# Kernel tuning notes

Hardware: AMD Instinct MI355X
Metric: run time of the kernel (lower is better)

## Reference

```python
import jax, jax.numpy as jnp
import numpy as np

N_NODES, N_EDGES, B, K, D = 200000, 500000, 8192, 32, 128
E_DIM, E_EMB, N_CLASS = 128, 128, 60


def setup_inputs() -> dict:
    key = jax.random.key(0)
    ks = jax.random.split(key, 16)
    s = lambda k, shape, scale=0.05: jax.random.normal(k, shape, dtype=jnp.float32) * scale
    return {
        'memory_emb': s(ks[0], (N_NODES, D), 1.0),
        'edge_feat': s(ks[1], (N_EDGES, E_DIM), 1.0),
        'W_q': s(ks[2], (D, D)),
        'W_k': s(ks[3], (D, D)),
        'a': s(ks[4], (2 * D,)),
        'We_w': s(ks[5], (E_DIM, E_EMB)),
        'We_b': s(ks[6], (E_EMB,)),
        'Wuc': s(ks[7], (D + 2 * D + E_EMB, D)),
        'Wc1': s(ks[8], (D, 128)),
        'Wc2': s(ks[9], (128, N_CLASS)),
        'src_idxs': jax.random.randint(ks[10], (B,), 0, N_NODES),
        'dst_idxs': jax.random.randint(ks[11], (B,), 0, N_NODES),
        'edge_idxs': jax.random.randint(ks[12], (B,), 0, N_EDGES),
        'src_neighbors': jax.random.randint(ks[13], (B, K), 0, N_NODES),
        'dst_neighbors': jax.random.randint(ks[14], (B, K), 0, N_NODES),
    }


def reference(memory_emb, edge_feat, W_q, W_k, a, We_w, We_b, Wuc, Wc1, Wc2,
              src_idxs, dst_idxs, edge_idxs, src_neighbors, dst_neighbors):
    def attend(idxs, nbrs):
        self_emb = memory_emb[idxs]                      # [B, D] gather
        nb = memory_emb[nbrs]                            # [B, K, D] gather
        q = self_emb @ W_q                               # [B, D]
        k = jnp.einsum('bkd,de->bke', nb, W_k)           # [B, K, D]
        # GAT-style score: leaky_relu(a . [q || k])
        sq = q @ a[:D]                                   # [B]
        sk = jnp.einsum('bkd,d->bk', k, a[D:])           # [B, K]
        score = jax.nn.leaky_relu(sq[:, None] + sk, 0.2)
        attn = jax.nn.softmax(score, axis=-1)            # [B, K]
        agg = jnp.einsum('bk,bkd->bd', attn, k)          # [B, D]
        return self_emb, agg

    src_e, src_h = attend(src_idxs, src_neighbors)
    dst_e, dst_h = attend(dst_idxs, dst_neighbors)
    e = edge_feat[edge_idxs] @ We_w + We_b               # edge embedding [B, E_EMB]
    msg_src = jax.nn.relu(jnp.concatenate([src_e, src_h, dst_h, e], -1) @ Wuc)
    msg_dst = jax.nn.relu(jnp.concatenate([dst_e, dst_h, src_h, e], -1) @ Wuc)
    logits_src = jax.nn.relu(msg_src @ Wc1) @ Wc2
    logits_dst = jax.nn.relu(msg_dst @ Wc1) @ Wc2
    return jnp.stack([logits_src, logits_dst])           # [2, B, N_CLASS]
```

## Files before the change

kernel.cpp:

```cpp
#include <hip/hip_runtime.h>

#define D 128
#define KNBR 32
#define BATCH 8192
#define NCLASS 60
#define NB 16
#define NP 32

__global__ __launch_bounds__(256) void k_prep(
    const float* __restrict__ Wq, const float* __restrict__ Wk,
    const float* __restrict__ a, const float* __restrict__ Wew,
    const float* __restrict__ Web, const float* __restrict__ Wuc,
    float* __restrict__ wqa, float* __restrict__ wka,
    float* __restrict__ be, float* __restrict__ Wcomb2)
{
    __shared__ float sB[128][129];
    int blk = blockIdx.x, tid = threadIdx.x;
    if (blk == 0) {
        for (int t = tid; t < 128 * 128; t += 256) sB[t >> 7][t & 127] = Wq[t];
        __syncthreads();
        if (tid < 128) {
            float s = 0.f;
            for (int j = 0; j < D; ++j) s += sB[tid][j] * a[j];
            wqa[tid] = s;
        }
        __syncthreads();
        for (int t = tid; t < 128 * 128; t += 256) sB[t >> 7][t & 127] = Wk[t];
        __syncthreads();
        if (tid < 128) {
            float s = 0.f;
            for (int j = 0; j < D; ++j) s += sB[tid][j] * a[D + j];
            wka[tid] = s;
        }
    } else if (blk == 1) {
        if (tid < 128) {
            float acc = 0.f;
            for (int j = 0; j < D; ++j) acc += Web[j] * Wuc[(size_t)(384 + j) * D + tid];
            be[tid] = acc;
        }
    } else {
        int g  = (blk - 2) >> 4;
        int rb = ((blk - 2) & 15) * 8;
        const float* A = (g == 2) ? Wew : Wk;
        const float* B = Wuc + (size_t)(128 + g * 128) * D;
        for (int t = tid; t < 128 * 128; t += 256) sB[t >> 7][t & 127] = B[t];
        __syncthreads();
        int j = tid & 127, half = tid >> 7;
        float acc[4] = {0.f, 0.f, 0.f, 0.f};
        int r0 = rb + half * 4;
        for (int t = 0; t < 128; ++t) {
            float bv = sB[t][j];
            #pragma unroll
            for (int m = 0; m < 4; ++m)
                acc[m] = fmaf(A[(size_t)(r0 + m) * D + t], bv, acc[m]);
        }
        #pragma unroll
        for (int m = 0; m < 4; ++m)
            Wcomb2[(size_t)(g * 128 + r0 + m) * D + j] = acc[m];
    }
}

__global__ __launch_bounds__(256) void k_scores(
    const float* __restrict__ mem,
    const float* __restrict__ wqa, const float* __restrict__ wka,
    float* __restrict__ nsq, float* __restrict__ nsk)
{
    int tid = threadIdx.x, lane = tid & 31, grp = tid >> 5;
    int n0 = blockIdx.x * 64 + grp * 8;
    float4 wq4 = ((const float4*)wqa)[lane];
    float4 wk4 = ((const float4*)wka)[lane];
    #pragma unroll
    for (int i = 0; i < 8; ++i) {
        int n = n0 + i;
        float4 v = ((const float4*)(mem + (size_t)n * D))[lane];
        float pq = v.x * wq4.x + v.y * wq4.y + v.z * wq4.z + v.w * wq4.w;
        float pk = v.x * wk4.x + v.y * wk4.y + v.z * wk4.z + v.w * wk4.w;
        #pragma unroll
        for (int m = 1; m <= 16; m <<= 1) {
            pq += __shfl_xor(pq, m, 32);
            pk += __shfl_xor(pk, m, 32);
        }
        if (lane == 0) nsq[n] = pq;
        if (lane == 1) nsk[n] = pk;
    }
}

__global__ __launch_bounds__(256, 3) void k_fused(
    const float* __restrict__ mem, const float* __restrict__ edge_feat,
    const float* __restrict__ Wuc, const float* __restrict__ Wcomb2,
    const float* __restrict__ be,
    const float* __restrict__ nsq, const float* __restrict__ nsk,
    const float* __restrict__ Wc1, const float* __restrict__ Wc2,
    const int* __restrict__ src_idxs, const int* __restrict__ dst_idxs,
    const int* __restrict__ edge_idxs,
    const int* __restrict__ src_nb, const int* __restrict__ dst_nb,
    float* __restrict__ out)
{
    __shared__ __align__(16) float Ws[32 * 128];
    __shared__ __align__(16) float nbT[128 * 33];
    __shared__ __align__(16) float uni[128 * 33];
    __shared__ int s_sidx[NP];
    __shared__ int s_eidx[NB];

    int tid = threadIdx.x;
    int b0 = blockIdx.x * NB;
    int lane = tid & 31;
    int grp  = tid >> 5;

    if (tid < NP) s_sidx[tid] = ((tid >> 4) ? dst_idxs : src_idxs)[b0 + (tid & 15)];
    if (tid < NB) s_eidx[tid] = edge_idxs[b0 + tid];

    for (int it = 0; it < 4; ++it) {
        int p = it * 8 + grp;
        int side = p >> 4;
        int bb = b0 + (p & 15);
        int self_idx = (side ? dst_idxs : src_idxs)[bb];
        int ik = (side ? dst_nb : src_nb)[(size_t)bb * KNBR + lane];

        float x = nsq[self_idx] + nsk[ik];
        x = (x >= 0.f) ? x : 0.2f * x;
        float mx = x;
        #pragma unroll
        for (int m = 1; m <= 16; m <<= 1) mx = fmaxf(mx, __shfl_xor(mx, m, 32));
        float e = __expf(x - mx);
        float sum = e;
        #pragma unroll
        for (int m = 1; m <= 16; m <<= 1) sum += __shfl_xor(sum, m, 32);
        float attn = e / sum;

        float4 acc = make_float4(0.f, 0.f, 0.f, 0.f);
        #pragma unroll 8
        for (int k = 0; k < KNBR; ++k) {
            int ikk  = __shfl(ik, k, 32);
            float ak = __shfl(attn, k, 32);
            float4 v = ((const float4*)(mem + (size_t)ikk * D))[lane];
            acc.x = fmaf(ak, v.x, acc.x);
            acc.y = fmaf(ak, v.y, acc.y);
            acc.z = fmaf(ak, v.z, acc.z);
            acc.w = fmaf(ak, v.w, acc.w);
        }
        nbT[(lane * 4 + 0) * 33 + p] = acc.x;
        nbT[(lane * 4 + 1) * 33 + p] = acc.y;
        nbT[(lane * 4 + 2) * 33 + p] = acc.z;
        nbT[(lane * 4 + 3) * 33 + p] = acc.w;
    }
    __syncthreads();

    int tr = tid >> 4, tc = tid & 15;
    int lc = tid & 31, lr = tid >> 5;
    int wc = tid & 127, wk2 = tid >> 7;
    float accB[2][8];
    #pragma unroll
    for (int i = 0; i < 2; ++i)
        #pragma unroll
        for (int j = 0; j < 8; ++j) accB[i][j] = 0.f;

    float* Ast = uni;

    for (int kt = 0; kt < 4; ++kt) {
        int off = kt * 32;
        #pragma unroll
        for (int q = 0; q < 4; ++q) {
            int r = lr + 8 * q;
            Ast[lc * 33 + r] = mem[(size_t)s_sidx[r] * D + off + lc];
        }
        #pragma unroll
        for (int pp = 0; pp < 16; ++pp) {
            int kk = wk2 + 2 * pp;
            Ws[kk * 128 + wc] = Wuc[(size_t)(off + kk) * D + wc];
        }
        __syncthreads();
        #pragma unroll 8
        for (int kk = 0; kk < 32; ++kk) {
            float a0 = Ast[kk * 33 + tr * 2];
            float a1 = Ast[kk * 33 + tr * 2 + 1];
            float4 w0 = *(const float4*)&Ws[kk * 128 + tc * 4];
            float4 w1 = *(const float4*)&Ws[kk * 128 + 64 + tc * 4];
            float wr[8] = {w0.x, w0.y, w0.z, w0.w, w1.x, w1.y, w1.z, w1.w};
            #pragma unroll
            for (int j = 0; j < 8; ++j) {
                accB[0][j] = fmaf(a0, wr[j], accB[0][j]);
                accB[1][j] = fmaf(a1, wr[j], accB[1][j]);
            }
        }
        __syncthreads();
    }
    for (int kt = 4; kt < 12; ++kt) {
        int off = (kt & 3) * 32;
        int gr0 = kt * 32 - 128;
        #pragma unroll
        for (int pp = 0; pp < 16; ++pp) {
            int kk = wk2 + 2 * pp;
            Ws[kk * 128 + wc] = Wcomb2[(size_t)(gr0 + kk) * D + wc];
        }
        __syncthreads();
        int r0 = (kt < 8) ? (tr * 2) : ((tr * 2) ^ 16);
        #pragma unroll 8
        for (int kk = 0; kk < 32; ++kk) {
            float a0 = nbT[(off + kk) * 33 + r0];
            float a1 = nbT[(off + kk) * 33 + r0 + 1];
            float4 w0 = *(const float4*)&Ws[kk * 128 + tc * 4];
            float4 w1 = *(const float4*)&Ws[kk * 128 + 64 + tc * 4];
            float wr[8] = {w0.x, w0.y, w0.z, w0.w, w1.x, w1.y, w1.z, w1.w};
            #pragma unroll
            for (int j = 0; j < 8; ++j) {
                accB[0][j] = fmaf(a0, wr[j], accB[0][j]);
                accB[1][j] = fmaf(a1, wr[j], accB[1][j]);
            }
        }
        __syncthreads();
    }
    for (int kt = 12; kt < 16; ++kt) {
        int off = (kt & 3) * 32;
        int gr0 = kt * 32 - 128;
        #pragma unroll
        for (int q = 0; q < 4; ++q) {
            int r = lr + 8 * q;
            Ast[lc * 33 + r] = edge_feat[(size_t)s_eidx[r & 15] * D + off + lc];
        }
        #pragma unroll
        for (int pp = 0; pp < 16; ++pp) {
            int kk = wk2 + 2 * pp;
            Ws[kk * 128 + wc] = Wcomb2[(size_t)(gr0 + kk) * D + wc];
        }
        __syncthreads();
        #pragma unroll 8
        for (int kk = 0; kk < 32; ++kk) {
            float a0 = Ast[kk * 33 + tr * 2];
            float a1 = Ast[kk * 33 + tr * 2 + 1];
            float4 w0 = *(const float4*)&Ws[kk * 128 + tc * 4];
            float4 w1 = *(const float4*)&Ws[kk * 128 + 64 + tc * 4];
            float wr[8] = {w0.x, w0.y, w0.z, w0.w, w1.x, w1.y, w1.z, w1.w};
            #pragma unroll
            for (int j = 0; j < 8; ++j) {
                accB[0][j] = fmaf(a0, wr[j], accB[0][j]);
                accB[1][j] = fmaf(a1, wr[j], accB[1][j]);
            }
        }
        __syncthreads();
    }

    float* msgT = uni;
    {
        float4 bv0 = *(const float4*)&be[tc * 4];
        float4 bv1 = *(const float4*)&be[64 + tc * 4];
        float b8[8] = {bv0.x, bv0.y, bv0.z, bv0.w, bv1.x, bv1.y, bv1.z, bv1.w};
        #pragma unroll
        for (int i = 0; i < 2; ++i) {
            int r = tr * 2 + i;
            #pragma unroll
            for (int j = 0; j < 4; ++j) {
                msgT[(tc * 4 + j) * 33 + r]      = fmaxf(accB[i][j] + b8[j], 0.f);
                msgT[(64 + tc * 4 + j) * 33 + r] = fmaxf(accB[i][j + 4] + b8[j + 4], 0.f);
            }
        }
    }
    __syncthreads();

    float accC[2][8];
    #pragma unroll
    for (int i = 0; i < 2; ++i)
        #pragma unroll
        for (int j = 0; j < 8; ++j) accC[i][j] = 0.f;

    for (int kt = 0; kt < 4; ++kt) {
        int off = kt * 32;
        #pragma unroll
        for (int pp = 0; pp < 16; ++pp) {
            int kk = wk2 + 2 * pp;
            Ws[kk * 128 + wc] = Wc1[(size_t)(off + kk) * D + wc];
        }
        __syncthreads();
        #pragma unroll 8
        for (int kk = 0; kk < 32; ++kk) {
            float a0 = msgT[(off + kk) * 33 + tr * 2];
            float a1 = msgT[(off + kk) * 33 + tr * 2 + 1];
            float4 w0 = *(const float4*)&Ws[kk * 128 + tc * 4];
            float4 w1 = *(const float4*)&Ws[kk * 128 + 64 + tc * 4];
            float wr[8] = {w0.x, w0.y, w0.z, w0.w, w1.x, w1.y, w1.z, w1.w};
            #pragma unroll
            for (int j = 0; j < 8; ++j) {
                accC[0][j] = fmaf(a0, wr[j], accC[0][j]);
                accC[1][j] = fmaf(a1, wr[j], accC[1][j]);
            }
        }
        __syncthreads();
    }
    #pragma unroll
    for (int i = 0; i < 2; ++i) {
        int r = tr * 2 + i;
        #pragma unroll
        for (int j = 0; j < 4; ++j) {
            msgT[(tc * 4 + j) * 33 + r]      = fmaxf(accC[i][j], 0.f);
            msgT[(64 + tc * 4 + j) * 33 + r] = fmaxf(accC[i][j + 4], 0.f);
        }
    }
    __syncthreads();

    int r2 = tid & 31;
    int cs = tid >> 5;
    float acc2[8];
    #pragma unroll
    for (int j = 0; j < 8; ++j) acc2[j] = 0.f;

    for (int kt = 0; kt < 4; ++kt) {
        int off = kt * 32;
        for (int t = tid; t < 32 * 64; t += 256) {
            int kk = t >> 6, c = t & 63;
            Ws[t] = (c < NCLASS) ? Wc2[(size_t)(off + kk) * NCLASS + c] : 0.f;
        }
        __syncthreads();
        #pragma unroll 4
        for (int kk = 0; kk < 32; ++kk) {
            float h = msgT[(off + kk) * 33 + r2];
            float4 w0 = *(const float4*)&Ws[kk * 64 + cs * 8];
            float4 w1 = *(const float4*)&Ws[kk * 64 + cs * 8 + 4];
            acc2[0] = fmaf(h, w0.x, acc2[0]);
            acc2[1] = fmaf(h, w0.y, acc2[1]);
            acc2[2] = fmaf(h, w0.z, acc2[2]);
            acc2[3] = fmaf(h, w0.w, acc2[3]);
            acc2[4] = fmaf(h, w1.x, acc2[4]);
            acc2[5] = fmaf(h, w1.y, acc2[5]);
            acc2[6] = fmaf(h, w1.z, acc2[6]);
            acc2[7] = fmaf(h, w1.w, acc2[7]);
        }
        __syncthreads();
    }
    {
        int side = r2 >> 4;
        int bb = b0 + (r2 & 15);
        size_t orow = ((size_t)side * BATCH + bb) * NCLASS;
        #pragma unroll
        for (int j = 0; j < 8; ++j) {
            int c = cs * 8 + j;
            if (c < NCLASS) out[orow + c] = acc2[j];
        }
    }
}

extern "C" void kernel_launch(void* const* d_in, const int* in_sizes, int n_in,
                              void* d_out, int out_size, void* d_ws, size_t ws_size,
                              hipStream_t stream) {
    const float* mem       = (const float*)d_in[0];
    const float* edge_feat = (const float*)d_in[1];
    const float* Wq        = (const float*)d_in[2];
    const float* Wk        = (const float*)d_in[3];
    const float* a         = (const float*)d_in[4];
    const float* Wew       = (const float*)d_in[5];
    const float* Web       = (const float*)d_in[6];
    const float* Wuc       = (const float*)d_in[7];
    const float* Wc1       = (const float*)d_in[8];
    const float* Wc2       = (const float*)d_in[9];
    const int* src_idxs    = (const int*)d_in[10];
    const int* dst_idxs    = (const int*)d_in[11];
    const int* edge_idxs   = (const int*)d_in[12];
    const int* src_nb      = (const int*)d_in[13];
    const int* dst_nb      = (const int*)d_in[14];
    float* out = (float*)d_out;

    float* ws = (float*)d_ws;
    float* Wcomb2 = ws;
    float* be     = ws + 49152;
    float* wqa    = ws + 49280;
    float* wka    = ws + 49408;
    float* nsq    = ws + 49536;
    float* nsk    = ws + 249536;

    k_prep<<<50, 256, 0, stream>>>(Wq, Wk, a, Wew, Web, Wuc, wqa, wka, be, Wcomb2);
    k_scores<<<200000 / 64, 256, 0, stream>>>(mem, wqa, wka, nsq, nsk);
    k_fused<<<BATCH / NB, 256, 0, stream>>>(mem, edge_feat, Wuc, Wcomb2, be,
                                            nsq, nsk, Wc1, Wc2,
                                            src_idxs, dst_idxs, edge_idxs,
                                            src_nb, dst_nb, out);
}
```

Baseline: 496.7 us.

## Split neighbor attention gather into a separate high-occupancy kernel

Moves the softmax attention and the weighted neighbor gather out of the fused GEMM kernel into a dedicated k_attn kernel. k_attn runs one 32-lane group per (side, batch) row across 2048 blocks and writes the aggregated vectors to a workspace buffer. The GEMM kernel then reads those vectors back instead of computing them. The goal is more memory-level parallelism for the latency-bound random gathers, which were limited by the fused kernel's 512 blocks and large shared-memory footprint. The cost is an extra launch plus a write and re-read of an 8 MB intermediate.

Result: no change. 501.0 us (+0.9%).

```diff
diff --git a/kernel.cpp b/kernel.cpp
--- a/kernel.cpp
+++ b/kernel.cpp
@@ -85,15 +85,54 @@
     }
 }
 
-__global__ __launch_bounds__(256, 3) void k_fused(
+__global__ __launch_bounds__(256) void k_attn(
+    const float* __restrict__ mem,
+    const float* __restrict__ nsq, const float* __restrict__ nsk,
+    const int* __restrict__ src_idxs, const int* __restrict__ dst_idxs,
+    const int* __restrict__ src_nb, const int* __restrict__ dst_nb,
+    float* __restrict__ agg)
+{
+    int lane = threadIdx.x & 31;
+    int grp  = threadIdx.x >> 5;
+    int p    = blockIdx.x * 8 + grp;
+    int side = p >> 13;
+    int b    = p & (BATCH - 1);
+
+    int self_idx = (side ? dst_idxs : src_idxs)[b];
+    int ik = (side ? dst_nb : src_nb)[(size_t)b * KNBR + lane];
+
+    float x = nsq[self_idx] + nsk[ik];
+    x = (x >= 0.f) ? x : 0.2f * x;
+    float mx = x;
+    #pragma unroll
+    for (int m = 1; m <= 16; m <<= 1) mx = fmaxf(mx, __shfl_xor(mx, m, 32));
+    float e = __expf(x - mx);
+    float s = e;
+    #pragma unroll
+    for (int m = 1; m <= 16; m <<= 1) s += __shfl_xor(s, m, 32);
+    float attn = e / s;
+
+    float4 acc = make_float4(0.f, 0.f, 0.f, 0.f);
+    #pragma unroll 8
+    for (int k = 0; k < KNBR; ++k) {
+        int   ikk = __shfl(ik, k, 32);
+        float ak  = __shfl(attn, k, 32);
+        float4 v = ((const float4*)(mem + (size_t)ikk * D))[lane];
+        acc.x = fmaf(ak, v.x, acc.x);
+        acc.y = fmaf(ak, v.y, acc.y);
+        acc.z = fmaf(ak, v.z, acc.z);
+        acc.w = fmaf(ak, v.w, acc.w);
+    }
+    ((float4*)(agg + (size_t)p * D))[lane] = acc;
+}
+
+__global__ __launch_bounds__(256, 3) void k_gemm(
     const float* __restrict__ mem, const float* __restrict__ edge_feat,
     const float* __restrict__ Wuc, const float* __restrict__ Wcomb2,
-    const float* __restrict__ be,
-    const float* __restrict__ nsq, const float* __restrict__ nsk,
+    const float* __restrict__ be, const float* __restrict__ agg,
     const float* __restrict__ Wc1, const float* __restrict__ Wc2,
     const int* __restrict__ src_idxs, const int* __restrict__ dst_idxs,
     const int* __restrict__ edge_idxs,
-    const int* __restrict__ src_nb, const int* __restrict__ dst_nb,
     float* __restrict__ out)
 {
     __shared__ __align__(16) float Ws[32 * 128];
@@ -110,39 +149,15 @@
     if (tid < NP) s_sidx[tid] = ((tid >> 4) ? dst_idxs : src_idxs)[b0 + (tid & 15)];
     if (tid < NB) s_eidx[tid] = edge_idxs[b0 + tid];
 
-    for (int it = 0; it < 4; ++it) {
-        int p = it * 8 + grp;
-        int side = p >> 4;
-        int bb = b0 + (p & 15);
-        int self_idx = (side ? dst_idxs : src_idxs)[bb];
-        int ik = (side ? dst_nb : src_nb)[(size_t)bb * KNBR + lane];
-
-        float x = nsq[self_idx] + nsk[ik];
-        x = (x >= 0.f) ? x : 0.2f * x;
-        float mx = x;
-        #pragma unroll
-        for (int m = 1; m <= 16; m <<= 1) mx = fmaxf(mx, __shfl_xor(mx, m, 32));
-        float e = __expf(x - mx);
-        float sum = e;
-        #pragma unroll
-        for (int m = 1; m <= 16; m <<= 1) sum += __shfl_xor(sum, m, 32);
-        float attn = e / sum;
-
-        float4 acc = make_float4(0.f, 0.f, 0.f, 0.f);
-        #pragma unroll 8
-        for (int k = 0; k < KNBR; ++k) {
-            int ikk  = __shfl(ik, k, 32);
-            float ak = __shfl(attn, k, 32);
-            float4 v = ((const float4*)(mem + (size_t)ikk * D))[lane];
-            acc.x = fmaf(ak, v.x, acc.x);
-            acc.y = fmaf(ak, v.y, acc.y);
-            acc.z = fmaf(ak, v.z, acc.z);
-            acc.w = fmaf(ak, v.w, acc.w);
-        }
-        nbT[(lane * 4 + 0) * 33 + p] = acc.x;
-        nbT[(lane * 4 + 1) * 33 + p] = acc.y;
-        nbT[(lane * 4 + 2) * 33 + p] = acc.z;
-        nbT[(lane * 4 + 3) * 33 + p] = acc.w;
+    #pragma unroll
+    for (int q = 0; q < 4; ++q) {
+        int pp = grp + 8 * q;
+        int gp = ((pp >> 4) ? BATCH : 0) + b0 + (pp & 15);
+        float4 v = ((const float4*)(agg + (size_t)gp * D))[lane];
+        nbT[(lane * 4 + 0) * 33 + pp] = v.x;
+        nbT[(lane * 4 + 1) * 33 + pp] = v.y;
+        nbT[(lane * 4 + 2) * 33 + pp] = v.z;
+        nbT[(lane * 4 + 3) * 33 + pp] = v.w;
     }
     __syncthreads();
 
@@ -365,11 +380,13 @@
     float* wka    = ws + 49408;
     float* nsq    = ws + 49536;
     float* nsk    = ws + 249536;
+    float* agg    = ws + 449536;
 
     k_prep<<<50, 256, 0, stream>>>(Wq, Wk, a, Wew, Web, Wuc, wqa, wka, be, Wcomb2);
     k_scores<<<200000 / 64, 256, 0, stream>>>(mem, wqa, wka, nsq, nsk);
-    k_fused<<<BATCH / NB, 256, 0, stream>>>(mem, edge_feat, Wuc, Wcomb2, be,
-                                            nsq, nsk, Wc1, Wc2,
-                                            src_idxs, dst_idxs, edge_idxs,
-                                            src_nb, dst_nb, out);
-}
+    k_attn<<<2 * BATCH / 8, 256, 0, stream>>>(mem, nsq, nsk, src_idxs, dst_idxs,
+                                              src_nb, dst_nb, agg);
+    k_gemm<<<BATCH / NB, 256, 0, stream>>>(mem, edge_feat, Wuc, Wcomb2, be, agg,
+                                           nsq ? Wc1 : Wc1, Wc2,
+                                           src_idxs, dst_idxs, edge_idxs, out);
+}
```
